# Performance work log

Measured on AMD Instinct MI355X. Metric: run time of the kernel, lower is better.

Reference implementation:

```python
import jax, jax.numpy as jnp
import numpy as np

TEMPERATURE = 0.1
NEG_INF = -1e30

def _normalize(v):
    # torch.nn.functional.normalize: v / max(||v||, 1e-12)
    n = jnp.linalg.norm(v, axis=-1, keepdims=True)
    return v / jnp.maximum(n, 1e-12)

def _line_loss(xn, yn, mx, my):
    # xn, yn: [T, D] normalized; mx, my: [T] {0,1} combined selection masks
    T = xn.shape[0]
    sim = (xn @ yn.T) / TEMPERATURE                     # [T, T]
    nx = jnp.sum(mx)
    ny = jnp.sum(my)
    # stable argsort puts selected indices first, preserving original order
    r = jnp.argsort(1 - mx)
    c = jnp.argsort(1 - my)
    sim_sel = sim[r][:, c]                              # selected block is top-left [nx, ny]
    ids = jnp.arange(T)
    masked = jnp.where((ids < nx)[:, None], sim_sel, NEG_INF)
    lse = jax.nn.logsumexp(masked, axis=0)              # column logsumexp over selected rows
    per = lse - jnp.diagonal(sim_sel)                   # = -log(exp(diag)/sum_col exp)
    m = jnp.minimum(nx, ny)                             # torch.diag length of [nx, ny] matrix
    return jnp.sum(jnp.where(ids < m, per, 0.0)) / m

def setup_inputs() -> dict:
    key = jax.random.key(0)
    k1, k2, k3, k4 = jax.random.split(key, 4)
    B, T, D = 8, 4096, 64
    x = jax.random.normal(k1, (B, T, D), dtype=jnp.float32)
    y = jax.random.normal(k2, (B, T, D), dtype=jnp.float32)
    image_masks1 = jax.random.randint(k3, (B, T), 0, 2).astype(jnp.int32)
    image_masks2 = jax.random.randint(k4, (B, T), 0, 2).astype(jnp.int32)
    shift_masks1 = jnp.ones((B, T), dtype=jnp.int32)
    shift_masks2 = jnp.ones((B, T), dtype=jnp.int32)
    return {"x": x, "y": y, "image_masks1": image_masks1, "image_masks2": image_masks2,
            "shift_masks1": shift_masks1, "shift_masks2": shift_masks2}

def reference(x, y, image_masks1, image_masks2, shift_masks1, shift_masks2):
    xn = _normalize(x)
    yn = _normalize(y)
    mx = shift_masks1 * image_masks1   # combined row selection (shift then image)
    my = shift_masks2 * image_masks2   # combined col selection
    losses = jax.vmap(_line_loss)(xn, yn, mx, my)  # [B]
    return jnp.mean(losses)
```

## Files before the change

kernel.cpp:

```cpp
#include <hip/hip_runtime.h>
#include <hip/hip_bf16.h>
#include <math.h>

#define T_DIM 4096
#define D_DIM 64
#define SPLITS 8
#define SCALE_X 14.4269504088896340736f
#define LN2 0.69314718055994530942f

typedef short bfrag8 __attribute__((ext_vector_type(8)));
typedef float floatx4 __attribute__((ext_vector_type(4)));

__device__ __forceinline__ float bf2f(unsigned short u) {
    return __uint_as_float(((unsigned int)u) << 16);
}

__launch_bounds__(256)
__global__ void prep(const float* __restrict__ x, const float* __restrict__ y,
                     const int* __restrict__ im1, const int* __restrict__ sh1,
                     const int* __restrict__ im2, const int* __restrict__ sh2,
                     __hip_bfloat16* __restrict__ xn, __hip_bfloat16* __restrict__ yn,
                     int* __restrict__ Ridx, int* __restrict__ Cidx,
                     int* __restrict__ cnt, float* __restrict__ gsum, float* __restrict__ out,
                     int rows, int normBlocks, int B) {
    int tid = threadIdx.x;
    if ((int)blockIdx.x < normBlocks) {
        int row = blockIdx.x * 16 + (tid >> 4);
        int l = tid & 15;
        const float* src; __hip_bfloat16* dst; float scale;
        if (row < rows) { src = x; dst = xn; scale = SCALE_X; }
        else { src = y; dst = yn; scale = 1.0f; row -= rows; }
        size_t off = (size_t)row * D_DIM + l * 4;
        float4 v = *reinterpret_cast<const float4*>(src + off);
        float ss = v.x * v.x + v.y * v.y + v.z * v.z + v.w * v.w;
        #pragma unroll
        for (int o = 1; o < 16; o <<= 1) ss += __shfl_xor(ss, o);
        float inv = scale / fmaxf(sqrtf(ss), 1e-12f);
        __hip_bfloat16 h0 = __float2bfloat16(v.x * inv);
        __hip_bfloat16 h1 = __float2bfloat16(v.y * inv);
        __hip_bfloat16 h2 = __float2bfloat16(v.z * inv);
        __hip_bfloat16 h3 = __float2bfloat16(v.w * inv);
        ushort4 o4;
        o4.x = *reinterpret_cast<unsigned short*>(&h0);
        o4.y = *reinterpret_cast<unsigned short*>(&h1);
        o4.z = *reinterpret_cast<unsigned short*>(&h2);
        o4.w = *reinterpret_cast<unsigned short*>(&h3);
        *reinterpret_cast<ushort4*>((unsigned short*)dst + off) = o4;
    } else {
        int z = blockIdx.x - normBlocks;
        int which = z & 1, b = z >> 1;
        const int* im = which ? im2 : im1;
        const int* sh = which ? sh2 : sh1;
        int* idxout   = which ? Cidx : Ridx;

        __shared__ int cw[64];
        __shared__ int offx[64];
        int w = tid >> 6, lane = tid & 63;
        const int* imb = im + (size_t)b * T_DIM;
        const int* shb = sh + (size_t)b * T_DIM;

        #pragma unroll
        for (int k = 0; k < 16; k++) {
            int u = w + k * 4;
            int t = u * 64 + lane;
            int mv = imb[t] * shb[t];
            unsigned long long bal = __ballot(mv != 0);
            if (lane == 0) cw[u] = __popcll(bal);
        }
        __syncthreads();
        if (w == 0) {
            int v = cw[lane];
            int incl = v;
            #pragma unroll
            for (int o = 1; o < 64; o <<= 1) {
                int t = __shfl_up(incl, o);
                if (lane >= o) incl += t;
            }
            offx[lane] = incl - v;
            if (lane == 63) cnt[which * B + b] = incl;
        }
        __syncthreads();
        #pragma unroll
        for (int k = 0; k < 16; k++) {
            int u = w + k * 4;
            int t = u * 64 + lane;
            int mv = imb[t] * shb[t];
            unsigned long long bal = __ballot(mv != 0);
            int pre = __popcll(bal & ((1ull << lane) - 1ull));
            if (mv) idxout[(size_t)b * T_DIM + offx[u] + pre] = t;
        }
        if (which == 0) {
            for (int i = tid; i < T_DIM; i += 256) gsum[(size_t)b * T_DIM + i] = 0.0f;
            if (b == 0 && tid == 0) out[0] = 0.0f;
        }
    }
}

__launch_bounds__(256)
__global__ void ntxent_main(const __hip_bfloat16* __restrict__ xn,
                            const __hip_bfloat16* __restrict__ yn,
                            const int* __restrict__ Ridx,
                            const int* __restrict__ Cidx,
                            const int* __restrict__ cnt,
                            float* __restrict__ gsum, int B) {
    int b  = blockIdx.y;
    int nx = cnt[b];
    int ny = cnt[B + b];
    int m  = min(nx, ny);
    int j0 = blockIdx.x * 64;
    if (j0 >= m) return;
    int rbase = blockIdx.z * 64;

    __shared__ __hip_bfloat16 Bs[64 * 72];
    __shared__ int Cloc[64];

    int tid  = threadIdx.x;
    int wave = tid >> 6, lane = tid & 63, quad = lane >> 4, c16 = lane & 15;

    if (tid < 64) {
        int j = j0 + tid;
        Cloc[tid] = (j < ny) ? Cidx[(size_t)b * T_DIM + j] : 0;
    }
    __syncthreads();

    #pragma unroll
    for (int i = tid; i < 64 * 8; i += 256) {
        int c = i >> 3, part = i & 7;
        bfrag8 v = *reinterpret_cast<const bfrag8*>(
            yn + ((size_t)b * T_DIM + Cloc[c]) * D_DIM + part * 8);
        *reinterpret_cast<bfrag8*>(&Bs[c * 72 + part * 8]) = v;
    }
    __syncthreads();

    bfrag8 bf[4][2];
    #pragma unroll
    for (int cg = 0; cg < 4; cg++)
        #pragma unroll
        for (int kh = 0; kh < 2; kh++)
            bf[cg][kh] = *reinterpret_cast<const bfrag8*>(
                &Bs[(cg * 16 + c16) * 72 + kh * 32 + quad * 8]);

    const __hip_bfloat16* xb = xn + (size_t)b * T_DIM * D_DIM;
    const int* Rb = Ridx + (size_t)b * T_DIM;

    float csum[4] = {0.f, 0.f, 0.f, 0.f};

    int gi = rbase + wave * 16 + c16;
    int idx0 = (gi < nx) ? Rb[gi] : 0;
    const __hip_bfloat16* arow = xb + (size_t)idx0 * D_DIM;
    bfrag8 af0 = *reinterpret_cast<const bfrag8*>(arow + quad * 8);
    bfrag8 af1 = *reinterpret_cast<const bfrag8*>(arow + 32 + quad * 8);

    for (int i0 = rbase; i0 < nx; i0 += 64 * SPLITS) {
        int gin = i0 + 64 * SPLITS + wave * 16 + c16;
        int idxn = (gin < nx) ? Rb[gin] : 0;
        const __hip_bfloat16* narow = xb + (size_t)idxn * D_DIM;
        bfrag8 naf0 = *reinterpret_cast<const bfrag8*>(narow + quad * 8);
        bfrag8 naf1 = *reinterpret_cast<const bfrag8*>(narow + 32 + quad * 8);

        int grow0 = i0 + wave * 16 + quad * 4;
        float wv[4];
        #pragma unroll
        for (int r = 0; r < 4; r++) wv[r] = (grow0 + r < nx) ? 1.0f : 0.0f;

        #pragma unroll
        for (int cg = 0; cg < 4; cg++) {
            floatx4 acc = {0.f, 0.f, 0.f, 0.f};
            acc = __builtin_amdgcn_mfma_f32_16x16x32_bf16(af0, bf[cg][0], acc, 0, 0, 0);
            acc = __builtin_amdgcn_mfma_f32_16x16x32_bf16(af1, bf[cg][1], acc, 0, 0, 0);
            #pragma unroll
            for (int r = 0; r < 4; r++)
                csum[cg] += wv[r] * exp2f(acc[r]);
        }
        af0 = naf0; af1 = naf1;
    }

    #pragma unroll
    for (int cg = 0; cg < 4; cg++) {
        csum[cg] += __shfl_xor(csum[cg], 16);
        csum[cg] += __shfl_xor(csum[cg], 32);
    }
    if (lane < 16) {
        #pragma unroll
        for (int cg = 0; cg < 4; cg++)
            atomicAdd(&gsum[(size_t)b * T_DIM + j0 + cg * 16 + c16], csum[cg]);
    }
}

__launch_bounds__(256)
__global__ void per_col_loss(const __hip_bfloat16* __restrict__ xn,
                             const __hip_bfloat16* __restrict__ yn,
                             const float* __restrict__ gsum,
                             const int* __restrict__ Ridx, const int* __restrict__ Cidx,
                             const int* __restrict__ cnt,
                             float* __restrict__ out, int B) {
    int b  = blockIdx.y;
    int m  = min(cnt[b], cnt[B + b]);
    if (m <= 0) return;

    int tid = threadIdx.x, wave = tid >> 6, lane = tid & 63;
    int g = tid >> 4, l = tid & 15;

    float acc = 0.0f;
    for (int j = blockIdx.x * 16 + g; j < m; j += 16 * gridDim.x) {
        int rj = Ridx[(size_t)b * T_DIM + j];
        int cj = Cidx[(size_t)b * T_DIM + j];
        const unsigned short* xa =
            (const unsigned short*)(xn + ((size_t)b * T_DIM + rj) * D_DIM) + l * 4;
        const unsigned short* yc =
            (const unsigned short*)(yn + ((size_t)b * T_DIM + cj) * D_DIM) + l * 4;
        float d = 0.0f;
        #pragma unroll
        for (int e = 0; e < 4; e++) d += bf2f(xa[e]) * bf2f(yc[e]);
        #pragma unroll
        for (int o = 1; o < 16; o <<= 1) d += __shfl_xor(d, o);
        if (l == 0) acc += LN2 * (__log2f(gsum[(size_t)b * T_DIM + j]) - d);
    }
    #pragma unroll
    for (int o = 1; o < 64; o <<= 1) acc += __shfl_xor(acc, o);
    __shared__ float ws[4];
    if (lane == 0) ws[wave] = acc;
    __syncthreads();
    if (tid == 0)
        atomicAdd(out, (ws[0] + ws[1] + ws[2] + ws[3]) / ((float)m * (float)B));
}

extern "C" void kernel_launch(void* const* d_in, const int* in_sizes, int n_in,
                              void* d_out, int out_size, void* d_ws, size_t ws_size,
                              hipStream_t stream) {
    const float* x  = (const float*)d_in[0];
    const float* y  = (const float*)d_in[1];
    const int* im1  = (const int*)d_in[2];
    const int* im2  = (const int*)d_in[3];
    const int* sh1  = (const int*)d_in[4];
    const int* sh2  = (const int*)d_in[5];

    int B = in_sizes[2] / T_DIM;
    int rows = B * T_DIM;
    size_t nElem = (size_t)rows * D_DIM;

    __hip_bfloat16* xn = (__hip_bfloat16*)d_ws;
    __hip_bfloat16* yn = xn + nElem;
    float* gsum = (float*)(yn + nElem);
    int*   Ridx = (int*)(gsum + rows);
    int*   Cidx = Ridx + rows;
    int*   cnt  = Cidx + rows;

    int normBlocks = 2 * rows / 16;
    prep<<<normBlocks + 2 * B, 256, 0, stream>>>(x, y, im1, sh1, im2, sh2,
                                                 xn, yn, Ridx, Cidx, cnt,
                                                 gsum, (float*)d_out, rows, normBlocks, B);

    dim3 grid(T_DIM / 64, B, SPLITS);
    ntxent_main<<<grid, 256, 0, stream>>>(xn, yn, Ridx, Cidx, cnt, gsum, B);

    dim3 grid2(16, B);
    per_col_loss<<<grid2, 256, 0, stream>>>(xn, yn, gsum, Ridx, Cidx, cnt,
                                            (float*)d_out, B);
}
```

Measured before the change: 108.4 us.

## Fuse per-column loss into main kernel via last-block completion counter

Removes the separate per_col_loss launch. Each main block bumps a per-(batch, column-tile) counter after its atomic gsum adds, and the last of the SPLITS blocks to finish computes the diagonal dot products, logs and loss contribution for its 64 columns. This saves one kernel launch and its dependency gap, in exchange for threadfences, an atomic counter per tile and a tail of extra work in the finishing blocks.

```diff
diff --git a/kernel.cpp b/kernel.cpp
--- a/kernel.cpp
+++ b/kernel.cpp
@@ -21,7 +21,8 @@
                      const int* __restrict__ im2, const int* __restrict__ sh2,
                      __hip_bfloat16* __restrict__ xn, __hip_bfloat16* __restrict__ yn,
                      int* __restrict__ Ridx, int* __restrict__ Cidx,
-                     int* __restrict__ cnt, float* __restrict__ gsum, float* __restrict__ out,
+                     int* __restrict__ cnt, float* __restrict__ gsum,
+                     int* __restrict__ done, float* __restrict__ out,
                      int rows, int normBlocks, int B) {
     int tid = threadIdx.x;
     if ((int)blockIdx.x < normBlocks) {
@@ -91,6 +92,7 @@
         }
         if (which == 0) {
             for (int i = tid; i < T_DIM; i += 256) gsum[(size_t)b * T_DIM + i] = 0.0f;
+            if (tid < 64) done[b * 64 + tid] = 0;
             if (b == 0 && tid == 0) out[0] = 0.0f;
         }
     }
@@ -102,7 +104,9 @@
                             const int* __restrict__ Ridx,
                             const int* __restrict__ Cidx,
                             const int* __restrict__ cnt,
-                            float* __restrict__ gsum, int B) {
+                            float* __restrict__ gsum,
+                            int* __restrict__ done,
+                            float* __restrict__ out, int B) {
     int b  = blockIdx.y;
     int nx = cnt[b];
     int ny = cnt[B + b];
@@ -141,7 +145,9 @@
                 &Bs[(cg * 16 + c16) * 72 + kh * 32 + quad * 8]);
 
     const __hip_bfloat16* xb = xn + (size_t)b * T_DIM * D_DIM;
+    const __hip_bfloat16* yb = yn + (size_t)b * T_DIM * D_DIM;
     const int* Rb = Ridx + (size_t)b * T_DIM;
+    const int* Cb = Cidx + (size_t)b * T_DIM;
 
     float csum[4] = {0.f, 0.f, 0.f, 0.f};
 
@@ -185,44 +191,47 @@
         for (int cg = 0; cg < 4; cg++)
             atomicAdd(&gsum[(size_t)b * T_DIM + j0 + cg * 16 + c16], csum[cg]);
     }
-}
-
-__launch_bounds__(256)
-__global__ void per_col_loss(const __hip_bfloat16* __restrict__ xn,
-                             const __hip_bfloat16* __restrict__ yn,
-                             const float* __restrict__ gsum,
-                             const int* __restrict__ Ridx, const int* __restrict__ Cidx,
-                             const int* __restrict__ cnt,
-                             float* __restrict__ out, int B) {
-    int b  = blockIdx.y;
-    int m  = min(cnt[b], cnt[B + b]);
-    if (m <= 0) return;
-
-    int tid = threadIdx.x, wave = tid >> 6, lane = tid & 63;
+
+    __threadfence();
+    __syncthreads();
+    __shared__ int amLast;
+    if (tid == 0) {
+        int old = atomicAdd(&done[b * 64 + blockIdx.x], 1);
+        amLast = (old == SPLITS - 1);
+    }
+    __syncthreads();
+    if (!amLast) return;
+    __threadfence();
+
     int g = tid >> 4, l = tid & 15;
-
     float acc = 0.0f;
-    for (int j = blockIdx.x * 16 + g; j < m; j += 16 * gridDim.x) {
-        int rj = Ridx[(size_t)b * T_DIM + j];
-        int cj = Cidx[(size_t)b * T_DIM + j];
-        const unsigned short* xa =
-            (const unsigned short*)(xn + ((size_t)b * T_DIM + rj) * D_DIM) + l * 4;
-        const unsigned short* yc =
-            (const unsigned short*)(yn + ((size_t)b * T_DIM + cj) * D_DIM) + l * 4;
-        float d = 0.0f;
-        #pragma unroll
-        for (int e = 0; e < 4; e++) d += bf2f(xa[e]) * bf2f(yc[e]);
-        #pragma unroll
-        for (int o = 1; o < 16; o <<= 1) d += __shfl_xor(d, o);
-        if (l == 0) acc += LN2 * (__log2f(gsum[(size_t)b * T_DIM + j]) - d);
+    #pragma unroll
+    for (int rep = 0; rep < 4; rep++) {
+        int j = j0 + g + rep * 16;
+        if (j < m) {
+            int rj = Rb[j];
+            int cj = Cb[j];
+            const unsigned short* xa = (const unsigned short*)(xb + (size_t)rj * D_DIM) + l * 4;
+            const unsigned short* yc = (const unsigned short*)(yb + (size_t)cj * D_DIM) + l * 4;
+            float d = 0.0f;
+            #pragma unroll
+            for (int e = 0; e < 4; e++) d += bf2f(xa[e]) * bf2f(yc[e]);
+            #pragma unroll
+            for (int o = 1; o < 16; o <<= 1) d += __shfl_xor(d, o);
+            if (l == 0) {
+                float gv = __hip_atomic_load(&gsum[(size_t)b * T_DIM + j],
+                                             __ATOMIC_ACQUIRE, __HIP_MEMORY_SCOPE_AGENT);
+                acc += LN2 * (__log2f(gv) - d);
+            }
+        }
     }
     #pragma unroll
     for (int o = 1; o < 64; o <<= 1) acc += __shfl_xor(acc, o);
-    __shared__ float ws[4];
-    if (lane == 0) ws[wave] = acc;
+    __shared__ float ws2[4];
+    if (lane == 0) ws2[wave] = acc;
     __syncthreads();
     if (tid == 0)
-        atomicAdd(out, (ws[0] + ws[1] + ws[2] + ws[3]) / ((float)m * (float)B));
+        atomicAdd(out, (ws2[0] + ws2[1] + ws2[2] + ws2[3]) / ((float)m * (float)B));
 }
 
 extern "C" void kernel_launch(void* const* d_in, const int* in_sizes, int n_in,
@@ -245,16 +254,15 @@
     int*   Ridx = (int*)(gsum + rows);
     int*   Cidx = Ridx + rows;
     int*   cnt  = Cidx + rows;
+    int*   done = cnt + 2 * B;
 
     int normBlocks = 2 * rows / 16;
     prep<<<normBlocks + 2 * B, 256, 0, stream>>>(x, y, im1, sh1, im2, sh2,
                                                  xn, yn, Ridx, Cidx, cnt,
-                                                 gsum, (float*)d_out, rows, normBlocks, B);
+                                                 gsum, done, (float*)d_out,
+                                                 rows, normBlocks, B);
 
     dim3 grid(T_DIM / 64, B, SPLITS);
-    ntxent_main<<<grid, 256, 0, stream>>>(xn, yn, Ridx, Cidx, cnt, gsum, B);
-
-    dim3 grid2(16, B);
-    per_col_loss<<<grid2, 256, 0, stream>>>(xn, yn, gsum, Ridx, Cidx, cnt,
-                                            (float*)d_out, B);
-}
+    ntxent_main<<<grid, 256, 0, stream>>>(xn, yn, Ridx, Cidx, cnt, gsum, done,
+                                          (float*)d_out, B);
+}
```

Measured after the change: 291.5 us. 2.69x slower.
